# Optimization experiments

Hardware: AMD Instinct MI355X
Metric: run time of the kernel (lower is better)

The kernel has to match this reference:

```python
import jax, jax.numpy as jnp
import numpy as np

INIT_W = 10.0
INIT_B = -5.0
N, M, D = 2048, 10, 256


def setup_inputs() -> dict:
    key = jax.random.key(0)
    k1, = jax.random.split(key, 1)
    embeddings = jax.random.normal(k1, (N, M, D), dtype=jnp.float32)
    w = jnp.asarray(INIT_W, dtype=jnp.float32)
    b = jnp.asarray(INIT_B, dtype=jnp.float32)
    return {"embeddings": embeddings, "w": w, "b": b}


def _l2norm(x, axis=-1, eps=1e-12):
    # matches torch F.normalize: x / max(||x||, eps)
    n = jnp.sqrt(jnp.sum(x * x, axis=axis, keepdims=True))
    return x / jnp.maximum(n, eps)


def reference(embeddings, w, b):
    # embeddings: (N, M, D)
    centroids = _l2norm(embeddings.mean(axis=1))          # (N, D)
    emb_norm = _l2norm(embeddings)                        # (N, M, D)
    sim = jnp.einsum('nmd,kd->nmk', emb_norm, centroids)  # (N, M, N)
    sim = sim * jnp.abs(w) + b
    # cross-entropy with target n for every (n, m):
    # loss = mean_{n,m} [ logsumexp_k sim[n,m,k] - sim[n,m,n] ]
    lse = jax.nn.logsumexp(sim, axis=-1)                  # (N, M)
    pos = jnp.take_along_axis(
        sim, jnp.arange(sim.shape[0])[:, None, None], axis=-1
    )[..., 0]                                             # (N, M)
    return jnp.mean(lse - pos)
```

## Files before the change

### kernel.cpp

```cpp
#include <hip/hip_runtime.h>
#include <hip/hip_bf16.h>

#define N_SPK 2048
#define M_UTT 10
#define D_DIM 256
#define NM (N_SPK * M_UTT)

typedef __attribute__((ext_vector_type(8))) short bf16x8_t;
typedef __attribute__((ext_vector_type(16))) float f32x16_t;

__device__ __forceinline__ short f2bf(float x) {
  __hip_bfloat16 h = __float2bfloat16(x);
  return *reinterpret_cast<short*>(&h);
}

__global__ __launch_bounds__(256) void k_prep(const float* __restrict__ emb,
                                              __hip_bfloat16* __restrict__ Bf,
                                              __hip_bfloat16* __restrict__ embn,
                                              float* __restrict__ dvals,
                                              float* __restrict__ rowsum,
                                              float* __restrict__ out) {
  const int n = blockIdx.x, d = threadIdx.x;
  const int wid = d >> 6, lane = d & 63;
  const float* p = emb + (size_t)n * (M_UTT * D_DIM) + d;

  float e[M_UTT];
  float s = 0.f;
#pragma unroll
  for (int m = 0; m < M_UTT; ++m) { e[m] = p[m * D_DIM]; s += e[m]; }

  float ss = s * s;
#pragma unroll
  for (int o = 32; o >= 1; o >>= 1) ss += __shfl_xor(ss, o, 64);
  __shared__ float redc[4];
  if (lane == 0) redc[wid] = ss;
  __syncthreads();
  float tot = redc[0] + redc[1] + redc[2] + redc[3];
  float inv = 1.0f / fmaxf(sqrtf(tot), 1e-11f);
  float v = s * inv;

  int idx = (((n >> 5) * 16 + (d >> 4)) * 64 + ((d >> 3) & 1) * 32 + (n & 31)) * 8 + (d & 7);
  Bf[idx] = __float2bfloat16(v);

  __shared__ float redm[M_UTT][2][4];
#pragma unroll
  for (int m = 0; m < M_UTT; ++m) {
    float a = e[m] * e[m], bb = e[m] * v;
#pragma unroll
    for (int o = 32; o >= 1; o >>= 1) {
      a += __shfl_xor(a, o, 64);
      bb += __shfl_xor(bb, o, 64);
    }
    if (lane == 0) { redm[m][0][wid] = a; redm[m][1][wid] = bb; }
  }
  __syncthreads();
  __shared__ float rnb[M_UTT];
  if (d < M_UTT) {
    float ssm = redm[d][0][0] + redm[d][0][1] + redm[d][0][2] + redm[d][0][3];
    float dtm = redm[d][1][0] + redm[d][1][1] + redm[d][1][2] + redm[d][1][3];
    float rn = 1.0f / fmaxf(sqrtf(ssm), 1e-12f);
    rnb[d] = rn;
    dvals[n * M_UTT + d] = dtm * rn;
    rowsum[n * M_UTT + d] = 0.f;
  }
  if (n == 0 && d == 0) out[0] = 0.f;
  __syncthreads();

  short* eo = (short*)embn;
#pragma unroll
  for (int m = 0; m < M_UTT; ++m) {
    int row = n * M_UTT + m;
    int u = (((row >> 5) * 16 + (d >> 4)) * 64 + ((d >> 3) & 1) * 32 + (row & 31));
    eo[u * 8 + (d & 7)] = f2bf(e[m] * rnb[m]);
  }
}

__global__ __launch_bounds__(512, 2) void k_gemm(const __hip_bfloat16* __restrict__ embn,
                                                 const __hip_bfloat16* __restrict__ Bf,
                                                 float* __restrict__ rowsum,
                                                 const float* __restrict__ wp) {
  const float aw = fabsf(wp[0]);
  const int tid = threadIdx.x;
  const int lane = tid & 63, w = tid >> 6;
  const int l31 = lane & 31;
  const int wr = w >> 1, wc = w & 1;
  const int row0 = blockIdx.y * 256 + wr * 64;
  const int cg0 = blockIdx.x * 4 + wc * 2;
  const int Rb = row0 >> 5;

  const bf16x8_t* bp0 = (const bf16x8_t*)Bf + (size_t)(cg0 * 16) * 64 + lane;
  const bf16x8_t* bp1 = (const bf16x8_t*)Bf + (size_t)((cg0 + 1) * 16) * 64 + lane;
  const bf16x8_t* fp = (const bf16x8_t*)embn;

  bf16x8_t cb0[3], cb1[3];
#pragma unroll
  for (int p = 0; p < 3; ++p) { cb0[p] = bp0[p * 64]; cb1[p] = bp1[p * 64]; }

  bf16x8_t breg[2][16];
#pragma unroll
  for (int rg = 0; rg < 2; ++rg)
#pragma unroll
    for (int ks = 0; ks < 16; ++ks)
      breg[rg][ks] = fp[(size_t)((Rb + rg) * 16 + ks) * 64 + lane];

  f32x16_t acc[2][2];
#pragma unroll
  for (int rg = 0; rg < 2; ++rg)
#pragma unroll
    for (int ci = 0; ci < 2; ++ci)
#pragma unroll
      for (int r = 0; r < 16; ++r) acc[rg][ci][r] = 0.f;

#pragma unroll
  for (int ks = 0; ks < 16; ++ks) {
    bf16x8_t b0 = cb0[ks % 3], b1 = cb1[ks % 3];
    if (ks + 3 < 16) {
      cb0[ks % 3] = bp0[(ks + 3) * 64];
      cb1[ks % 3] = bp1[(ks + 3) * 64];
    }
    acc[0][0] = __builtin_amdgcn_mfma_f32_32x32x16_bf16(b0, breg[0][ks], acc[0][0], 0, 0, 0);
    acc[0][1] = __builtin_amdgcn_mfma_f32_32x32x16_bf16(b1, breg[0][ks], acc[0][1], 0, 0, 0);
    acc[1][0] = __builtin_amdgcn_mfma_f32_32x32x16_bf16(b0, breg[1][ks], acc[1][0], 0, 0, 0);
    acc[1][1] = __builtin_amdgcn_mfma_f32_32x32x16_bf16(b1, breg[1][ks], acc[1][1], 0, 0, 0);
  }

#pragma unroll
  for (int rg = 0; rg < 2; ++rg) {
    float s = 0.f;
#pragma unroll
    for (int ci = 0; ci < 2; ++ci)
#pragma unroll
      for (int r = 0; r < 16; ++r)
        s += __expf(fmaf(aw, acc[rg][ci][r], -aw));
    s += __shfl_xor(s, 32, 64);
    if (lane < 32) atomicAdd(&rowsum[row0 + rg * 32 + lane], s);
  }
}

__global__ __launch_bounds__(256) void k_final(const float* __restrict__ rowsum,
                                               const float* __restrict__ dvals,
                                               const float* __restrict__ wp,
                                               float* __restrict__ out) {
  const float aw = fabsf(wp[0]);
  int base = blockIdx.x * 512 + threadIdx.x;
  float c = 0.f;
#pragma unroll
  for (int j = 0; j < 2; ++j) {
    int r = base + j * 256;
    c += logf(rowsum[r]) + aw * (1.0f - dvals[r]);
  }
#pragma unroll
  for (int o = 32; o >= 1; o >>= 1) c += __shfl_xor(c, o, 64);
  __shared__ float rs[4];
  int wid = threadIdx.x >> 6, lane = threadIdx.x & 63;
  if (lane == 0) rs[wid] = c;
  __syncthreads();
  if (threadIdx.x == 0)
    atomicAdd(out, (rs[0] + rs[1] + rs[2] + rs[3]) * (1.0f / (float)NM));
}

extern "C" void kernel_launch(void* const* d_in, const int* in_sizes, int n_in,
                              void* d_out, int out_size, void* d_ws, size_t ws_size,
                              hipStream_t stream) {
  const float* emb = (const float*)d_in[0];
  const float* wp  = (const float*)d_in[1];
  float* out = (float*)d_out;

  char* ws = (char*)d_ws;
  float* rowsum = (float*)(ws);
  float* dvals  = (float*)(ws + (128 << 10));
  __hip_bfloat16* Bf   = (__hip_bfloat16*)(ws + (1 << 20));
  __hip_bfloat16* embn = (__hip_bfloat16*)(ws + (2 << 20));

  k_prep<<<N_SPK, 256, 0, stream>>>(emb, Bf, embn, dvals, rowsum, out);
  k_gemm<<<dim3(16, NM / 256), 512, 0, stream>>>(embn, Bf, rowsum, wp);
  k_final<<<NM / 512, 256, 0, stream>>>(rowsum, dvals, wp, out);
}
```

Baseline: 116.1 us.

## Stage centroid tile in LDS via global_load_lds and loop column groups per wave

The GEMM kernel now uses 256-thread blocks where each of four waves owns 64 rows and iterates over the block's four 32-column centroid groups (two passes of two). The block's full 128x256 bf16 centroid tile is loaded once into shared memory with direct global-to-LDS loads, so it is no longer streamed per-wave from global memory. This aims to cut redundant global/L2 traffic for the B operand and to amortise each wave's register-resident embedding fragments over more columns. The costs are 64KB of LDS per block, which may limit occupancy, plus a full-barrier wait before any compute starts and LDS read traffic in the inner loop.

```diff
diff --git a/kernel.cpp b/kernel.cpp
--- a/kernel.cpp
+++ b/kernel.cpp
@@ -75,27 +75,30 @@
   }
 }
 
-__global__ __launch_bounds__(512, 2) void k_gemm(const __hip_bfloat16* __restrict__ embn,
+__global__ __launch_bounds__(256, 2) void k_gemm(const __hip_bfloat16* __restrict__ embn,
                                                  const __hip_bfloat16* __restrict__ Bf,
                                                  float* __restrict__ rowsum,
                                                  const float* __restrict__ wp) {
+  __shared__ short Bs[128 * 256];
   const float aw = fabsf(wp[0]);
   const int tid = threadIdx.x;
   const int lane = tid & 63, w = tid >> 6;
   const int l31 = lane & 31;
-  const int wr = w >> 1, wc = w & 1;
-  const int row0 = blockIdx.y * 256 + wr * 64;
-  const int cg0 = blockIdx.x * 4 + wc * 2;
-  const int Rb = row0 >> 5;
+  const int row0 = blockIdx.y * 256 + w * 64;
+  const int Rb = blockIdx.y * 8 + w * 2;
 
-  const bf16x8_t* bp0 = (const bf16x8_t*)Bf + (size_t)(cg0 * 16) * 64 + lane;
-  const bf16x8_t* bp1 = (const bf16x8_t*)Bf + (size_t)((cg0 + 1) * 16) * 64 + lane;
+  {
+    const short* src = (const short*)Bf + (size_t)blockIdx.x * 32768 + w * 512 + lane * 8;
+#pragma unroll
+    for (int it = 0; it < 16; ++it) {
+      __builtin_amdgcn_global_load_lds(
+          (const __attribute__((address_space(1))) void*)(src + it * 2048),
+          (__attribute__((address_space(3))) void*)&Bs[it * 2048 + w * 512],
+          16, 0, 0);
+    }
+  }
+
   const bf16x8_t* fp = (const bf16x8_t*)embn;
-
-  bf16x8_t cb0[3], cb1[3];
-#pragma unroll
-  for (int p = 0; p < 3; ++p) { cb0[p] = bp0[p * 64]; cb1[p] = bp1[p * 64]; }
-
   bf16x8_t breg[2][16];
 #pragma unroll
   for (int rg = 0; rg < 2; ++rg)
@@ -103,36 +106,46 @@
     for (int ks = 0; ks < 16; ++ks)
       breg[rg][ks] = fp[(size_t)((Rb + rg) * 16 + ks) * 64 + lane];
 
-  f32x16_t acc[2][2];
-#pragma unroll
-  for (int rg = 0; rg < 2; ++rg)
-#pragma unroll
-    for (int ci = 0; ci < 2; ++ci)
-#pragma unroll
-      for (int r = 0; r < 16; ++r) acc[rg][ci][r] = 0.f;
+  asm volatile("s_waitcnt vmcnt(0)" ::: "memory");
+  __syncthreads();
+
+  float rowacc[2] = {0.f, 0.f};
 
 #pragma unroll
-  for (int ks = 0; ks < 16; ++ks) {
-    bf16x8_t b0 = cb0[ks % 3], b1 = cb1[ks % 3];
-    if (ks + 3 < 16) {
-      cb0[ks % 3] = bp0[(ks + 3) * 64];
-      cb1[ks % 3] = bp1[(ks + 3) * 64];
+  for (int c = 0; c < 2; ++c) {
+    f32x16_t acc[2][2];
+#pragma unroll
+    for (int rg = 0; rg < 2; ++rg)
+#pragma unroll
+      for (int ci = 0; ci < 2; ++ci)
+#pragma unroll
+        for (int r = 0; r < 16; ++r) acc[rg][ci][r] = 0.f;
+
+#pragma unroll
+    for (int ks = 0; ks < 16; ++ks) {
+      bf16x8_t c0 = *(const bf16x8_t*)&Bs[((2 * c) * 16 + ks) * 512 + lane * 8];
+      bf16x8_t c1 = *(const bf16x8_t*)&Bs[((2 * c + 1) * 16 + ks) * 512 + lane * 8];
+      acc[0][0] = __builtin_amdgcn_mfma_f32_32x32x16_bf16(c0, breg[0][ks], acc[0][0], 0, 0, 0);
+      acc[0][1] = __builtin_amdgcn_mfma_f32_32x32x16_bf16(c1, breg[0][ks], acc[0][1], 0, 0, 0);
+      acc[1][0] = __builtin_amdgcn_mfma_f32_32x32x16_bf16(c0, breg[1][ks], acc[1][0], 0, 0, 0);
+      acc[1][1] = __builtin_amdgcn_mfma_f32_32x32x16_bf16(c1, breg[1][ks], acc[1][1], 0, 0, 0);
     }
-    acc[0][0] = __builtin_amdgcn_mfma_f32_32x32x16_bf16(b0, breg[0][ks], acc[0][0], 0, 0, 0);
-    acc[0][1] = __builtin_amdgcn_mfma_f32_32x32x16_bf16(b1, breg[0][ks], acc[0][1], 0, 0, 0);
-    acc[1][0] = __builtin_amdgcn_mfma_f32_32x32x16_bf16(b0, breg[1][ks], acc[1][0], 0, 0, 0);
-    acc[1][1] = __builtin_amdgcn_mfma_f32_32x32x16_bf16(b1, breg[1][ks], acc[1][1], 0, 0, 0);
+
+#pragma unroll
+    for (int rg = 0; rg < 2; ++rg) {
+      float s = 0.f;
+#pragma unroll
+      for (int ci = 0; ci < 2; ++ci)
+#pragma unroll
+        for (int r = 0; r < 16; ++r)
+          s += __expf(fmaf(aw, acc[rg][ci][r], -aw));
+      rowacc[rg] += s;
+    }
   }
 
 #pragma unroll
   for (int rg = 0; rg < 2; ++rg) {
-    float s = 0.f;
-#pragma unroll
-    for (int ci = 0; ci < 2; ++ci)
-#pragma unroll
-      for (int r = 0; r < 16; ++r)
-        s += __expf(fmaf(aw, acc[rg][ci][r], -aw));
-    s += __shfl_xor(s, 32, 64);
+    float s = rowacc[rg] + __shfl_xor(rowacc[rg], 32, 64);
     if (lane < 32) atomicAdd(&rowsum[row0 + rg * 32 + lane], s);
   }
 }
@@ -173,6 +186,6 @@
   __hip_bfloat16* embn = (__hip_bfloat16*)(ws + (2 << 20));
 
   k_prep<<<N_SPK, 256, 0, stream>>>(emb, Bf, embn, dvals, rowsum, out);
-  k_gemm<<<dim3(16, NM / 256), 512, 0, stream>>>(embn, Bf, rowsum, wp);
+  k_gemm<<<dim3(16, NM / 256), 256, 0, stream>>>(embn, Bf, rowsum, wp);
   k_final<<<NM / 512, 256, 0, stream>>>(rowsum, dvals, wp, out);
 }
```

Result: faster. 108.0 us (-6.9%).
